# Kernel tuning notes

Hardware: AMD Instinct MI355X
Metric: run time of the kernel (lower is better)

## Reference

```python
import jax, jax.numpy as jnp
import numpy as np

NEG_SLOPE = 0.1  # negative slope of LeakyReLU in Conv3dReLU/Conv2dReLU


def setup_inputs() -> dict:
    key = jax.random.key(0)
    ks = jax.random.split(key, 16)
    B, C, PREV, N, M1, M2 = 2, 16, 16, 16384, 4096, 4096
    D1, CORR, FILT = 4, 15, 15          # d1 = d+1; (r+1)^d1 - r^d1 with r=1
    CO0, CO1 = 32, 32                    # num_corr_output
    O0, O1 = 64, 64                      # num_output
    CIN = 2 * C + PREV                   # corr_conv input channels

    feat1 = jax.random.normal(ks[0], (B, C, M1), jnp.float32)
    feat2 = jax.random.normal(ks[1], (B, C, M2), jnp.float32)
    prev_corr_feat = jax.random.normal(ks[2], (B, PREV, N), jnp.float32)
    barycentric1 = jax.random.uniform(ks[3], (B, D1, N), jnp.float32)
    # lattice_offset1: batch-offset flattened indices into [0, B*(M1+1)); value -1+1=0 is the pad slot
    local = jax.random.randint(ks[4], (B, D1, N), 0, M1)
    lattice_offset1 = local + (jnp.arange(B, dtype=jnp.int64) * (M1 + 1))[:, None, None]
    pc1_corr_indices = jax.random.randint(ks[5], (B, CORR, M1), -1, M1).astype(jnp.int64)
    pc2_corr_indices = jax.random.randint(ks[6], (B, FILT, CORR, M1), -1, M2).astype(jnp.int64)

    s = 0.05
    cw0 = jax.random.normal(ks[7], (CO0, CIN, CORR), jnp.float32) * s   # Conv3d (1,corr_size,1)
    cb0 = jax.random.normal(ks[8], (CO0,), jnp.float32) * s
    cw1 = jax.random.normal(ks[9], (CO1, CO0), jnp.float32) * s        # Conv3d 1x1x1
    cb1 = jax.random.normal(ks[10], (CO1,), jnp.float32) * s
    bw0 = jax.random.normal(ks[11], (O0, CO1, FILT), jnp.float32) * s  # Conv2d (filter_size,1)
    bb0 = jax.random.normal(ks[12], (O0,), jnp.float32) * s
    bw1 = jax.random.normal(ks[13], (O1, O0), jnp.float32) * s         # Conv2d 1x1 (no relu)
    bb1 = jax.random.normal(ks[14], (O1,), jnp.float32) * s

    return {
        "feat1": feat1, "feat2": feat2, "prev_corr_feat": prev_corr_feat,
        "barycentric1": barycentric1,
        "cw0": cw0, "cb0": cb0, "cw1": cw1, "cb1": cb1,
        "bw0": bw0, "bb0": bb0, "bw1": bw1, "bb1": bb1,
        "lattice_offset1": lattice_offset1,
        "pc1_corr_indices": pc1_corr_indices,
        "pc2_corr_indices": pc2_corr_indices,
        "max_hash_cnt1": M1, "max_hash_cnt2": M2,
    }


def reference(feat1, feat2, prev_corr_feat, barycentric1,
              cw0, cb0, cw1, cb1, bw0, bb0, bw1, bb1,
              lattice_offset1, pc1_corr_indices, pc2_corr_indices,
              max_hash_cnt1, max_hash_cnt2):
    B, C, M1 = feat1.shape
    PREV = prev_corr_feat.shape[1]

    # ---- splat prev_corr_feat onto lattice vertices (scatter-add) ----
    flat_idx = (lattice_offset1 + 1).reshape(-1)                      # (B*d1*N,)
    # (B, PREV, d1, N) -> (B, d1, N, PREV) -> (B*d1*N, PREV)
    vals = (barycentric1[:, None, :, :] * prev_corr_feat[:, :, None, :])
    vals = vals.transpose(0, 2, 3, 1).reshape(-1, PREV)
    prev_splat = jax.ops.segment_sum(vals, flat_idx, num_segments=B * (M1 + 1))
    prev_splat = prev_splat.reshape(B, M1 + 1, PREV).transpose(0, 2, 1)  # (B, PREV, M1+1)

    # use_norm: normalize by splatted barycentric mass
    ones_splat = jax.ops.segment_sum(barycentric1.reshape(-1), flat_idx,
                                     num_segments=B * (M1 + 1)).reshape(B, M1 + 1)
    prev_splat = prev_splat * (1.0 / (ones_splat + 1e-5))[:, None, :]

    # ---- prepend zero pad slot (index 0 catches -1 neighbor indices) ----
    splat1 = jnp.concatenate([prev_splat, jnp.pad(feat1, ((0, 0), (0, 0), (1, 0)))], axis=1)  # (B, PREV+C, M1+1)
    splat2 = jnp.pad(feat2, ((0, 0), (0, 0), (1, 0)))                                          # (B, C, M2+1)

    # ---- irregular gathers ----
    g1 = jax.vmap(lambda s, i: s[:, i])(splat1, pc1_corr_indices + 1)   # (B, PREV+C, corr, M1)
    g2 = jax.vmap(lambda s, i: s[:, i])(splat2, pc2_corr_indices + 1)   # (B, C, filt, corr, M1)
    FILT = g2.shape[2]
    g1b = jnp.broadcast_to(g1[:, :, None], (B, g1.shape[1], FILT, g1.shape[2], M1))
    combined = jnp.concatenate([g1b, g2], axis=1)                       # (B, 2C+PREV, filt, corr, M1)

    # ---- corr_conv: Conv3d(1,corr,1)+LeakyReLU, then 1x1x1+LeakyReLU ----
    x = jnp.einsum('bifkn,oik->bofn', combined, cw0) + cb0[None, :, None, None]
    x = jax.nn.leaky_relu(x, NEG_SLOPE)
    x = jnp.einsum('bcfn,oc->bofn', x, cw1) + cb1[None, :, None, None]
    x = jax.nn.leaky_relu(x, NEG_SLOPE)

    # ---- blur_conv: Conv2d(filt,1)+LeakyReLU, then 1x1 (last_relu=False) ----
    y = jnp.einsum('bcfn,ocf->bon', x, bw0) + bb0[None, :, None]
    y = jax.nn.leaky_relu(y, NEG_SLOPE)
    y = jnp.einsum('bcn,oc->bon', y, bw1) + bb1[None, :, None]
    return y
```

## Files before the change

### kernel.cpp

```cpp
#include <hip/hip_runtime.h>
#include <hip/hip_bf16.h>

namespace {

constexpr int B     = 2;
constexpr int C     = 16;
constexpr int PREVC = 16;
constexpr int NPTS  = 16384;
constexpr int M1    = 4096;
constexpr int D1    = 4;
constexpr int CORR  = 15;
constexpr int FILT  = 15;
constexpr int CIN   = 48;
constexpr int CO0   = 32;
constexpr int O1    = 64;
constexpr int MS    = M1 + 1;
constexpr int NSLOT = B * MS;
constexpr int NPAIR = B * D1 * NPTS;
constexpr int BCAP  = 64;
constexpr int GSTR  = 240;
constexpr float NEG = 0.1f;

constexpr size_t OFF_SP1   = 0;
constexpr size_t SZ_SP1    = (size_t)NSLOT * 32;
constexpr size_t OFF_SP2   = OFF_SP1 + SZ_SP1;
constexpr size_t SZ_SP2    = (size_t)NSLOT * 16;
constexpr size_t OFF_P     = OFF_SP2 + SZ_SP2;
constexpr size_t SZ_PQ     = (size_t)B * CORR * MS * 32 / 2;
constexpr size_t OFF_Q     = OFF_P + SZ_PQ;
constexpr size_t OFF_CWT   = OFF_Q + SZ_PQ;
constexpr size_t SZ_CWT    = (size_t)CORR * CIN * 32;
constexpr size_t OFF_W0R   = OFF_CWT + SZ_CWT;
constexpr size_t SZ_W0R    = 512 * 64;
constexpr size_t OFF_H     = OFF_W0R + SZ_W0R;
constexpr size_t SZ_H      = (size_t)B * M1 * 512 / 2;
constexpr size_t OFF_PREVT = OFF_H + SZ_H;
constexpr size_t SZ_PREVT  = (size_t)B * NPTS * 16;
constexpr size_t OFF_CNT   = OFF_PREVT + SZ_PREVT;
constexpr size_t SZ_CNT    = 8208;
constexpr size_t OFF_REC   = OFF_CNT + SZ_CNT;
constexpr size_t SZ_REC    = (size_t)NSLOT * BCAP;
constexpr size_t OFF_GT    = OFF_REC + SZ_REC;
constexpr size_t SZ_GT     = (size_t)B * M1 * GSTR;

__device__ __forceinline__ float leaky(float v) { return v > 0.f ? v : NEG * v; }
__device__ __forceinline__ float bflo(unsigned u) { return __uint_as_float(u << 16); }
__device__ __forceinline__ float bfhi(unsigned u) { return __uint_as_float(u & 0xffff0000u); }

__global__ __launch_bounds__(256) void k_pre(const int* __restrict__ lo,
                                             const float* __restrict__ prev,
                                             const float* __restrict__ cw0,
                                             const float* __restrict__ bw0,
                                             const int* __restrict__ pc1,
                                             const int* __restrict__ pc2,
                                             int* __restrict__ counts,
                                             int* __restrict__ rec,
                                             float* __restrict__ prevT,
                                             float* __restrict__ cwT,
                                             float* __restrict__ W0r,
                                             unsigned int* __restrict__ gT) {
  int bx = blockIdx.x, tid = threadIdx.x;
  if (bx < 512) {
    int t = bx * 256 + tid;
    int slot = lo[t] + 1;
    int pos = atomicAdd(counts + slot, 1);
    if (pos < BCAP) rec[slot * BCAP + pos] = t;
  } else if (bx < 1024) {
    __shared__ float tile[16][65];
    int bb = bx - 512;
    int b = bb >> 8, n0 = (bb & 255) * 64;
    for (int e = tid; e < 1024; e += 256) {
      int ln = e & 63, r = e >> 6;
      tile[r][ln] = prev[((size_t)b * PREVC + r) * NPTS + n0 + ln];
    }
    __syncthreads();
    for (int e = tid; e < 1024; e += 256) {
      int c = e & 15, nn = e >> 4;
      prevT[((size_t)b * NPTS + n0 + nn) * 16 + c] = tile[c][nn];
    }
  } else if (bx < 1243) {
    int e = (bx - 1024) * 256 + tid;
    if (e < CORR * CIN * 32) {
      int o = e & 31, i = (e >> 5) % CIN, k = e / (CIN * 32);
      cwT[e] = cw0[((size_t)o * CIN + i) * CORR + k];
    }
    int e2 = e - CORR * CIN * 32;
    if (e2 >= 0 && e2 < 512 * 64) {
      int o3 = e2 & 63, cf = e2 >> 6, c = cf >> 4, f = cf & 15;
      W0r[e2] = (f < FILT) ? bw0[((size_t)o3 * CO0 + c) * FILT + f] : 0.f;
    }
  } else {
    __shared__ int tile[16][65];
    int t = bx - 1243;
    int n0 = (t & 63) * 64;
    int rest = t >> 6;
    int b = rest & 1;
    int rt = rest >> 1;
    const int* src; int r0, nr, doff;
    if (rt < 15) { src = pc2 + (size_t)b * FILT * CORR * M1; r0 = rt * 16;
                   nr = min(16, FILT * CORR - r0); doff = 0; }
    else         { src = pc1 + (size_t)b * CORR * M1; r0 = 0; nr = CORR; doff = 225; }
    for (int e = tid; e < nr * 64; e += 256) {
      int ln = e & 63, r = e >> 6;
      tile[r][ln] = src[(size_t)(r0 + r) * M1 + n0 + ln] + 1;
    }
    __syncthreads();
    for (int e = tid; e < 1024; e += 256) {
      int rr = e & 15, nn = e >> 4;
      if (rr < nr)
        gT[((size_t)b * M1 + n0 + nn) * GSTR + doff + r0 + rr] =
            (unsigned int)(tile[rr][nn] * 64);
    }
  }
}

__global__ __launch_bounds__(256) void k_sum(const int* __restrict__ rec,
                                             const int* __restrict__ counts,
                                             const float* __restrict__ bary,
                                             const float* __restrict__ prevT,
                                             const float* __restrict__ feat1,
                                             const float* __restrict__ feat2,
                                             float* __restrict__ splat1,
                                             float* __restrict__ splat2) {
  int tid = threadIdx.x;
  int s = blockIdx.x * 4 + (tid >> 6);
  if (s >= NSLOT) return;
  int lane = tid & 63, c = lane & 15, g = lane >> 4;
  int cnt = min(counts[s], BCAP);
  const int* bucket = rec + (size_t)s * BCAP;
  float acc = 0.f, wsum = 0.f;
  for (int e = g; e < cnt; e += 4) {
    int t = bucket[e];
    float w = bary[t];
    int n = t & (NPTS - 1);
    int b = t >> 16;
    acc += w * prevT[((size_t)b * NPTS + n) * 16 + c];
    wsum += w;
  }
  acc  += __shfl_down(acc, 32);  acc  += __shfl_down(acc, 16);
  wsum += __shfl_down(wsum, 32); wsum += __shfl_down(wsum, 16);
  if (lane < 16) {
    int m = s % MS, b2 = s / MS;
    float scale = 1.f / (wsum + 1e-5f);
    splat1[(size_t)s * 32 + c] = acc * scale;
    float f1 = (m == 0) ? 0.f : feat1[((size_t)b2 * C + c) * M1 + (m - 1)];
    splat1[(size_t)s * 32 + 16 + c] = f1;
    float f2 = (m == 0) ? 0.f : feat2[((size_t)b2 * C + c) * M1 + (m - 1)];
    splat2[(size_t)s * 16 + c] = f2;
  }
}

__global__ __launch_bounds__(256) void k_pq(const float* __restrict__ sp1,
                                            const float* __restrict__ sp2,
                                            const float* __restrict__ cwT,
                                            __hip_bfloat16* __restrict__ Pt,
                                            __hip_bfloat16* __restrict__ Qt) {
  __shared__ float wk[CIN][33];
  int k = blockIdx.y, b = blockIdx.z;
  int tid = threadIdx.x;
  int m = blockIdx.x * 16 + (tid >> 4);
  int o2 = tid & 15;
  for (int e = tid; e < CIN * 32; e += 256)
    wk[e >> 5][e & 31] = cwT[(size_t)k * CIN * 32 + e];
  __syncthreads();
  if (m >= MS) return;
  const float* s1 = sp1 + ((size_t)b * MS + m) * 32;
  const float* s2 = sp2 + ((size_t)b * MS + m) * 16;
  int oa = o2 * 2, ob = oa + 1;
  float q0 = 0, q1 = 0, p0 = 0, p1 = 0;
#pragma unroll
  for (int i4 = 0; i4 < 8; ++i4) {
    float4 s = *(const float4*)(s1 + i4 * 4);
    q0 += s.x * wk[i4*4+0][oa] + s.y * wk[i4*4+1][oa] + s.z * wk[i4*4+2][oa] + s.w * wk[i4*4+3][oa];
    q1 += s.x * wk[i4*4+0][ob] + s.y * wk[i4*4+1][ob] + s.z * wk[i4*4+2][ob] + s.w * wk[i4*4+3][ob];
  }
#pragma unroll
  for (int i4 = 0; i4 < 4; ++i4) {
    float4 s = *(const float4*)(s2 + i4 * 4);
    p0 += s.x * wk[32+i4*4+0][oa] + s.y * wk[32+i4*4+1][oa] + s.z * wk[32+i4*4+2][oa] + s.w * wk[32+i4*4+3][oa];
    p1 += s.x * wk[32+i4*4+0][ob] + s.y * wk[32+i4*4+1][ob] + s.z * wk[32+i4*4+2][ob] + s.w * wk[32+i4*4+3][ob];
  }
  size_t base = ((size_t)(b * CORR + k) * MS + m) * 32;
  __hip_bfloat162 qq, pp;
  qq.x = __float2bfloat16(q0); qq.y = __float2bfloat16(q1);
  pp.x = __float2bfloat16(p0); pp.y = __float2bfloat16(p1);
  *reinterpret_cast<__hip_bfloat162*>(Qt + base + oa) = qq;
  *reinterpret_cast<__hip_bfloat162*>(Pt + base + oa) = pp;
}

__global__ __launch_bounds__(256) void k_gather(const __hip_bfloat16* __restrict__ Pt,
                                                const __hip_bfloat16* __restrict__ Qt,
                                                const unsigned int* __restrict__ gT,
                                                const float* __restrict__ cw1,
                                                const float* __restrict__ cb0,
                                                const float* __restrict__ cb1,
                                                __hip_bfloat16* __restrict__ hbuf) {
  __shared__ unsigned int idxs[4][GSTR];
  __shared__ float p1s[4][32];
  __shared__ float xls[4][16][33];

  int bid = blockIdx.x;
  int b = (bid >> 2) & 1;
  int r = bid & 3, x = bid >> 3;
  int n0 = (r << 10) | (x << 2);
  int pt0 = (b << 12) | n0;
  int tid = threadIdx.x;

  for (int e = tid; e < 240; e += 256) {
    int pl = e / 60, d = e - pl * 60;
    ((uint4*)idxs[pl])[d] =
        ((const uint4*)(gT + (size_t)(pt0 + pl) * GSTR))[d];
  }
  __syncthreads();

  int pl = tid >> 6, lane = tid & 63;
  int f = lane >> 2, o4 = lane & 3;

  {
    const char* base = (const char*)((f < CORR ? Pt : Qt) + (size_t)b * CORR * MS * 32);
    const unsigned int* ip = &idxs[pl][f < CORR ? f * CORR : 225];
    unsigned int lo = (unsigned int)(o4 * 16);
    float a[8] = {};
#pragma unroll
    for (int k = 0; k < CORR; ++k) {
      unsigned int off = ip[k] + (unsigned int)(k * MS * 64) + lo;
      uint4 d = *(const uint4*)(base + off);
      a[0] += bflo(d.x); a[1] += bfhi(d.x);
      a[2] += bflo(d.y); a[3] += bfhi(d.y);
      a[4] += bflo(d.z); a[5] += bfhi(d.z);
      a[6] += bflo(d.w); a[7] += bfhi(d.w);
    }
    if (f == CORR) {
#pragma unroll
      for (int j = 0; j < 8; ++j)
        p1s[pl][o4 * 8 + j] = a[j] + cb0[o4 * 8 + j];
    }
    __syncthreads();
    if (f < CORR) {
#pragma unroll
      for (int j = 0; j < 8; ++j)
        xls[pl][f][o4 * 8 + j] = leaky(a[j] + p1s[pl][o4 * 8 + j]);
    }
  }
  __syncthreads();

  {
    int o = lane & 31, fh = lane >> 5;
    const float* wrow = cw1 + o * CO0;
    float bias = cb1[o];
    float h[8];
#pragma unroll
    for (int j = 0; j < 8; ++j) {
      float hh = bias;
#pragma unroll
      for (int c4 = 0; c4 < 8; ++c4) {
        float4 xv = *(const float4*)&xls[pl][fh * 8 + j][c4 * 4];
        float4 w  = *(const float4*)(wrow + c4 * 4);
        hh += w.x * xv.x + w.y * xv.y + w.z * xv.z + w.w * xv.w;
      }
      h[j] = leaky(hh);
    }
    if (fh == 1) h[7] = 0.f;
    union { __hip_bfloat16 hb[8]; uint4 u; } pk;
#pragma unroll
    for (int j = 0; j < 8; ++j) pk.hb[j] = __float2bfloat16(h[j]);
    *(uint4*)(hbuf + (size_t)(pt0 + pl) * 512 + o * 16 + fh * 8) = pk.u;
  }
}

__global__ __launch_bounds__(256) void k_blur(const __hip_bfloat16* __restrict__ hbuf,
                                              const float* __restrict__ W0r,
                                              const float* __restrict__ bb0,
                                              const float* __restrict__ bw1,
                                              const float* __restrict__ bb1,
                                              float* __restrict__ out) {
  __shared__ float hs[64][33];
  __shared__ float ws[64][68];
  __shared__ float y0s[64][36];

  int bid = blockIdx.x;
  int b = bid >> 7;
  int n0 = (bid & 127) * 32;
  int tid = threadIdx.x;
  int og = tid & 15, ng = tid >> 4;

  float acc[4][2] = {};
  for (int kc = 0; kc < 512; kc += 64) {
    __syncthreads();
    {
      int nn = tid >> 3, k8 = tid & 7;
      const __hip_bfloat16* hp = hbuf + ((size_t)b * M1 + n0 + nn) * 512 + kc + k8 * 8;
#pragma unroll
      for (int j = 0; j < 4; ++j) {
        __hip_bfloat162 v2 = *(const __hip_bfloat162*)(hp + j * 2);
        hs[k8 * 8 + j * 2 + 0][nn] = __bfloat162float(v2.x);
        hs[k8 * 8 + j * 2 + 1][nn] = __bfloat162float(v2.y);
      }
    }
    for (int e = tid; e < 1024; e += 256) {
      int row = e >> 4, c4 = e & 15;
      *(float4*)&ws[row][c4 * 4] = *(const float4*)(W0r + (size_t)(kc + row) * 64 + c4 * 4);
    }
    __syncthreads();
#pragma unroll 16
    for (int kk = 0; kk < 64; ++kk) {
      float4 w = *(const float4*)&ws[kk][og * 4];
      float h0 = hs[kk][ng * 2], h1 = hs[kk][ng * 2 + 1];
      acc[0][0] += w.x * h0; acc[0][1] += w.x * h1;
      acc[1][0] += w.y * h0; acc[1][1] += w.y * h1;
      acc[2][0] += w.z * h0; acc[2][1] += w.z * h1;
      acc[3][0] += w.w * h0; acc[3][1] += w.w * h1;
    }
  }
  __syncthreads();

#pragma unroll
  for (int i = 0; i < 4; ++i) {
    int o3 = og * 4 + i;
    float bias = bb0[o3];
#pragma unroll
    for (int j = 0; j < 2; ++j)
      y0s[o3][ng * 2 + j] = leaky(acc[i][j] + bias);
  }
  for (int e = tid; e < 64 * 64; e += 256) {
    int o1e = e >> 6, c = e & 63;
    ws[c][o1e] = bw1[e];
  }
  __syncthreads();

  int o1 = tid & 63, ng4 = tid >> 6;
  float a8[8] = {};
  for (int c = 0; c < 64; ++c) {
    float w = ws[c][o1];
    float4 ya = *(const float4*)&y0s[c][ng4 * 8];
    float4 yb = *(const float4*)&y0s[c][ng4 * 8 + 4];
    a8[0] += w * ya.x; a8[1] += w * ya.y; a8[2] += w * ya.z; a8[3] += w * ya.w;
    a8[4] += w * yb.x; a8[5] += w * yb.y; a8[6] += w * yb.z; a8[7] += w * yb.w;
  }
  float bias = bb1[o1];
#pragma unroll
  for (int j = 0; j < 8; ++j)
    out[((size_t)b * O1 + o1) * M1 + n0 + ng4 * 8 + j] = a8[j] + bias;
}

}

extern "C" void kernel_launch(void* const* d_in, const int* in_sizes, int n_in,
                              void* d_out, int out_size, void* d_ws, size_t ws_size,
                              hipStream_t stream) {
  const float* feat1 = (const float*)d_in[0];
  const float* feat2 = (const float*)d_in[1];
  const float* prev  = (const float*)d_in[2];
  const float* bary  = (const float*)d_in[3];
  const float* cw0   = (const float*)d_in[4];
  const float* cb0   = (const float*)d_in[5];
  const float* cw1   = (const float*)d_in[6];
  const float* cb1   = (const float*)d_in[7];
  const float* bw0   = (const float*)d_in[8];
  const float* bb0   = (const float*)d_in[9];
  const float* bw1   = (const float*)d_in[10];
  const float* bb1   = (const float*)d_in[11];
  const int* lo  = (const int*)d_in[12];
  const int* pc1 = (const int*)d_in[13];
  const int* pc2 = (const int*)d_in[14];

  float* ws = (float*)d_ws;
  float* splat1 = ws + OFF_SP1;
  float* splat2 = ws + OFF_SP2;
  __hip_bfloat16* Pt = (__hip_bfloat16*)(ws + OFF_P);
  __hip_bfloat16* Qt = (__hip_bfloat16*)(ws + OFF_Q);
  float* cwT   = ws + OFF_CWT;
  float* W0r   = ws + OFF_W0R;
  __hip_bfloat16* hbuf = (__hip_bfloat16*)(ws + OFF_H);
  float* prevT = ws + OFF_PREVT;
  int* counts  = (int*)(ws + OFF_CNT);
  int* rec     = (int*)(ws + OFF_REC);
  unsigned int* gT = (unsigned int*)(ws + OFF_GT);
  float* out   = (float*)d_out;

  hipMemsetAsync(counts, 0, NSLOT * sizeof(int), stream);

  hipLaunchKernelGGL(k_pre, dim3(1243 + 2048), dim3(256), 0, stream,
                     lo, prev, cw0, bw0, pc1, pc2, counts, rec, prevT, cwT, W0r, gT);
  hipLaunchKernelGGL(k_sum, dim3((NSLOT + 3) / 4), dim3(256), 0, stream,
                     rec, counts, bary, prevT, feat1, feat2, splat1, splat2);
  hipLaunchKernelGGL(k_pq, dim3((MS + 15) / 16, CORR, B), dim3(256), 0, stream,
                     splat1, splat2, cwT, Pt, Qt);
  hipLaunchKernelGGL(k_gather, dim3(B * M1 / 4), dim3(256), 0, stream,
                     Pt, Qt, gT, cw1, cb0, cb1, hbuf);
  hipLaunchKernelGGL(k_blur, dim3(B * M1 / 32), dim3(256), 0, stream,
                     hbuf, W0r, bb0, bw1, bb1, out);
}
```

Baseline: 124.1 us.

## Fuse blur convolution into gather kernel, eliminating the hbuf intermediate

Merges the k_blur stage into k_gather. Each 4-point block now keeps its 512-wide hidden vector in shared memory in bf16, then computes the filter-size conv and the 1x1 output conv in place. This removes the global hbuf write and read and one kernel launch. In exchange, every block streams the full 128 KB W0r weight matrix through shared memory in 16 chunks with a sync each, which is far more redundant L2 traffic than the old 32-point blur blocks. Output stores are also only 4 floats wide, and a new occupancy hint of 8 blocks per CU may raise register pressure.

```diff
diff --git a/kernel.cpp b/kernel.cpp
--- a/kernel.cpp
+++ b/kernel.cpp
@@ -32,9 +32,7 @@
 constexpr size_t SZ_CWT    = (size_t)CORR * CIN * 32;
 constexpr size_t OFF_W0R   = OFF_CWT + SZ_CWT;
 constexpr size_t SZ_W0R    = 512 * 64;
-constexpr size_t OFF_H     = OFF_W0R + SZ_W0R;
-constexpr size_t SZ_H      = (size_t)B * M1 * 512 / 2;
-constexpr size_t OFF_PREVT = OFF_H + SZ_H;
+constexpr size_t OFF_PREVT = OFF_W0R + SZ_W0R;
 constexpr size_t SZ_PREVT  = (size_t)B * NPTS * 16;
 constexpr size_t OFF_CNT   = OFF_PREVT + SZ_PREVT;
 constexpr size_t SZ_CNT    = 8208;
@@ -188,16 +186,25 @@
   *reinterpret_cast<__hip_bfloat162*>(Pt + base + oa) = pp;
 }
 
-__global__ __launch_bounds__(256) void k_gather(const __hip_bfloat16* __restrict__ Pt,
-                                                const __hip_bfloat16* __restrict__ Qt,
-                                                const unsigned int* __restrict__ gT,
-                                                const float* __restrict__ cw1,
-                                                const float* __restrict__ cb0,
-                                                const float* __restrict__ cb1,
-                                                __hip_bfloat16* __restrict__ hbuf) {
-  __shared__ unsigned int idxs[4][GSTR];
-  __shared__ float p1s[4][32];
-  __shared__ float xls[4][16][33];
+__global__ __launch_bounds__(256, 8) void k_gather(const __hip_bfloat16* __restrict__ Pt,
+                                                   const __hip_bfloat16* __restrict__ Qt,
+                                                   const unsigned int* __restrict__ gT,
+                                                   const float* __restrict__ cw1,
+                                                   const float* __restrict__ cb0,
+                                                   const float* __restrict__ cb1,
+                                                   const float* __restrict__ W0r,
+                                                   const float* __restrict__ bb0,
+                                                   const float* __restrict__ bw1,
+                                                   const float* __restrict__ bb1,
+                                                   float* __restrict__ out) {
+  __shared__ __attribute__((aligned(16))) char smem[19008];
+  unsigned int* idxs = (unsigned int*)smem;
+  float* parts       = (float*)smem;
+  float* p1s         = (float*)(smem + 4096);
+  float* xls         = (float*)(smem + 4608);
+  float* wch         = (float*)(smem + 4608);
+  __hip_bfloat16* hT = (__hip_bfloat16*)(smem + 13824);
+  float* y0s         = (float*)(smem + 17920);
 
   int bid = blockIdx.x;
   int b = (bid >> 2) & 1;
@@ -208,17 +215,17 @@
 
   for (int e = tid; e < 240; e += 256) {
     int pl = e / 60, d = e - pl * 60;
-    ((uint4*)idxs[pl])[d] =
+    ((uint4*)(idxs + pl * GSTR))[d] =
         ((const uint4*)(gT + (size_t)(pt0 + pl) * GSTR))[d];
   }
   __syncthreads();
 
   int pl = tid >> 6, lane = tid & 63;
-  int f = lane >> 2, o4 = lane & 3;
 
   {
+    int f = lane >> 2, o4 = lane & 3;
     const char* base = (const char*)((f < CORR ? Pt : Qt) + (size_t)b * CORR * MS * 32);
-    const unsigned int* ip = &idxs[pl][f < CORR ? f * CORR : 225];
+    const unsigned int* ip = idxs + pl * GSTR + (f < CORR ? f * CORR : 225);
     unsigned int lo = (unsigned int)(o4 * 16);
     float a[8] = {};
 #pragma unroll
@@ -233,13 +240,13 @@
     if (f == CORR) {
 #pragma unroll
       for (int j = 0; j < 8; ++j)
-        p1s[pl][o4 * 8 + j] = a[j] + cb0[o4 * 8 + j];
+        p1s[pl * 32 + o4 * 8 + j] = a[j] + cb0[o4 * 8 + j];
     }
     __syncthreads();
     if (f < CORR) {
 #pragma unroll
       for (int j = 0; j < 8; ++j)
-        xls[pl][f][o4 * 8 + j] = leaky(a[j] + p1s[pl][o4 * 8 + j]);
+        xls[pl * 576 + f * 36 + o4 * 8 + j] = leaky(a[j] + p1s[pl * 32 + o4 * 8 + j]);
     }
   }
   __syncthreads();
@@ -254,7 +261,7 @@
       float hh = bias;
 #pragma unroll
       for (int c4 = 0; c4 < 8; ++c4) {
-        float4 xv = *(const float4*)&xls[pl][fh * 8 + j][c4 * 4];
+        float4 xv = *(const float4*)&xls[pl * 576 + (fh * 8 + j) * 36 + c4 * 4];
         float4 w  = *(const float4*)(wrow + c4 * 4);
         hh += w.x * xv.x + w.y * xv.y + w.z * xv.z + w.w * xv.w;
       }
@@ -264,83 +271,53 @@
     union { __hip_bfloat16 hb[8]; uint4 u; } pk;
 #pragma unroll
     for (int j = 0; j < 8; ++j) pk.hb[j] = __float2bfloat16(h[j]);
-    *(uint4*)(hbuf + (size_t)(pt0 + pl) * 512 + o * 16 + fh * 8) = pk.u;
-  }
-}
-
-__global__ __launch_bounds__(256) void k_blur(const __hip_bfloat16* __restrict__ hbuf,
-                                              const float* __restrict__ W0r,
-                                              const float* __restrict__ bb0,
-                                              const float* __restrict__ bw1,
-                                              const float* __restrict__ bb1,
-                                              float* __restrict__ out) {
-  __shared__ float hs[64][33];
-  __shared__ float ws[64][68];
-  __shared__ float y0s[64][36];
-
-  int bid = blockIdx.x;
-  int b = bid >> 7;
-  int n0 = (bid & 127) * 32;
-  int tid = threadIdx.x;
-  int og = tid & 15, ng = tid >> 4;
-
-  float acc[4][2] = {};
-  for (int kc = 0; kc < 512; kc += 64) {
-    __syncthreads();
-    {
-      int nn = tid >> 3, k8 = tid & 7;
-      const __hip_bfloat16* hp = hbuf + ((size_t)b * M1 + n0 + nn) * 512 + kc + k8 * 8;
-#pragma unroll
-      for (int j = 0; j < 4; ++j) {
-        __hip_bfloat162 v2 = *(const __hip_bfloat162*)(hp + j * 2);
-        hs[k8 * 8 + j * 2 + 0][nn] = __bfloat162float(v2.x);
-        hs[k8 * 8 + j * 2 + 1][nn] = __bfloat162float(v2.y);
-      }
-    }
-    for (int e = tid; e < 1024; e += 256) {
-      int row = e >> 4, c4 = e & 15;
-      *(float4*)&ws[row][c4 * 4] = *(const float4*)(W0r + (size_t)(kc + row) * 64 + c4 * 4);
-    }
-    __syncthreads();
-#pragma unroll 16
-    for (int kk = 0; kk < 64; ++kk) {
-      float4 w = *(const float4*)&ws[kk][og * 4];
-      float h0 = hs[kk][ng * 2], h1 = hs[kk][ng * 2 + 1];
-      acc[0][0] += w.x * h0; acc[0][1] += w.x * h1;
-      acc[1][0] += w.y * h0; acc[1][1] += w.y * h1;
-      acc[2][0] += w.z * h0; acc[2][1] += w.z * h1;
-      acc[3][0] += w.w * h0; acc[3][1] += w.w * h1;
-    }
-  }
-  __syncthreads();
-
-#pragma unroll
-  for (int i = 0; i < 4; ++i) {
-    int o3 = og * 4 + i;
-    float bias = bb0[o3];
-#pragma unroll
-    for (int j = 0; j < 2; ++j)
-      y0s[o3][ng * 2 + j] = leaky(acc[i][j] + bias);
-  }
-  for (int e = tid; e < 64 * 64; e += 256) {
-    int o1e = e >> 6, c = e & 63;
-    ws[c][o1e] = bw1[e];
-  }
-  __syncthreads();
-
-  int o1 = tid & 63, ng4 = tid >> 6;
-  float a8[8] = {};
-  for (int c = 0; c < 64; ++c) {
-    float w = ws[c][o1];
-    float4 ya = *(const float4*)&y0s[c][ng4 * 8];
-    float4 yb = *(const float4*)&y0s[c][ng4 * 8 + 4];
-    a8[0] += w * ya.x; a8[1] += w * ya.y; a8[2] += w * ya.z; a8[3] += w * ya.w;
-    a8[4] += w * yb.x; a8[5] += w * yb.y; a8[6] += w * yb.z; a8[7] += w * yb.w;
-  }
-  float bias = bb1[o1];
-#pragma unroll
-  for (int j = 0; j < 8; ++j)
-    out[((size_t)b * O1 + o1) * M1 + n0 + ng4 * 8 + j] = a8[j] + bias;
+    *(uint4*)(hT + pl * 512 + o * 16 + fh * 8) = pk.u;
+  }
+
+  int og = tid & 15, bpl = (tid >> 4) & 3, rep = tid >> 6;
+  float acc[4] = {};
+  for (int kc = 0; kc < 512; kc += 32) {
+    __syncthreads();
+    for (int e = tid; e < 512; e += 256) {
+      int rr = e >> 4, c4 = e & 15;
+      *(float4*)&wch[rr * 68 + c4 * 4] = *(const float4*)(W0r + (size_t)(kc + rr) * 64 + c4 * 4);
+    }
+    __syncthreads();
+#pragma unroll
+    for (int i = 0; i < 8; ++i) {
+      int kk = rep + i * 4;
+      float hv = __bfloat162float(hT[bpl * 512 + kc + kk]);
+      float4 w = *(const float4*)&wch[kk * 68 + og * 4];
+      acc[0] += w.x * hv; acc[1] += w.y * hv; acc[2] += w.z * hv; acc[3] += w.w * hv;
+    }
+  }
+  __syncthreads();
+  *(float4*)&parts[((rep * 4 + bpl) * 16 + og) * 4] = make_float4(acc[0], acc[1], acc[2], acc[3]);
+  __syncthreads();
+
+  {
+    int ypl = tid & 3, yo3 = tid >> 2;
+    int og2 = yo3 >> 2, comp = yo3 & 3;
+    float y0 = bb0[yo3];
+#pragma unroll
+    for (int rp = 0; rp < 4; ++rp)
+      y0 += parts[((rp * 4 + ypl) * 16 + og2) * 4 + comp];
+    y0s[ypl * 68 + yo3] = leaky(y0);
+  }
+  __syncthreads();
+
+  {
+    int fpl = tid & 3, fo1 = tid >> 2;
+    const float* w1row = bw1 + fo1 * 64;
+    float y1 = bb1[fo1];
+#pragma unroll
+    for (int c4 = 0; c4 < 16; ++c4) {
+      float4 w = *(const float4*)(w1row + c4 * 4);
+      y1 += w.x * y0s[fpl * 68 + c4 * 4 + 0] + w.y * y0s[fpl * 68 + c4 * 4 + 1] +
+            w.z * y0s[fpl * 68 + c4 * 4 + 2] + w.w * y0s[fpl * 68 + c4 * 4 + 3];
+    }
+    out[((size_t)(b * O1 + fo1)) * M1 + n0 + fpl] = y1;
+  }
 }
 
 }
@@ -371,7 +348,6 @@
   __hip_bfloat16* Qt = (__hip_bfloat16*)(ws + OFF_Q);
   float* cwT   = ws + OFF_CWT;
   float* W0r   = ws + OFF_W0R;
-  __hip_bfloat16* hbuf = (__hip_bfloat16*)(ws + OFF_H);
   float* prevT = ws + OFF_PREVT;
   int* counts  = (int*)(ws + OFF_CNT);
   int* rec     = (int*)(ws + OFF_REC);
@@ -387,7 +363,5 @@
   hipLaunchKernelGGL(k_pq, dim3((MS + 15) / 16, CORR, B), dim3(256), 0, stream,
                      splat1, splat2, cwT, Pt, Qt);
   hipLaunchKernelGGL(k_gather, dim3(B * M1 / 4), dim3(256), 0, stream,
-                     Pt, Qt, gT, cw1, cb0, cb1, hbuf);
-  hipLaunchKernelGGL(k_blur, dim3(B * M1 / 32), dim3(256), 0, stream,
-                     hbuf, W0r, bb0, bw1, bb1, out);
-}
+                     Pt, Qt, gT, cw1, cb0, cb1, W0r, bb0, bw1, bb1, out);
+}
```

Measured after the change: 123.6 us. About the same (-0.4%).
